# Kernel tuning notes

Hardware: AMD Instinct MI355X
Metric: run time of the kernel (lower is better)

Reference implementation:

```python
import jax, jax.numpy as jnp
import numpy as np

ROPE_BASE = 1000.0  # note: module uses base=1000, not the usual 10000


def _rope(x):
    # x: [B, L, H, d]; rotates the full head dim (x_pass is empty since d == hid_head)
    d = x.shape[-1]
    L = x.shape[1]
    theta = 1.0 / (ROPE_BASE ** (jnp.arange(0, d, 2, dtype=jnp.float32) / d))  # [d/2]
    idx = jnp.arange(L, dtype=jnp.float32)[:, None] * theta[None, :]            # [L, d/2]
    idx2 = jnp.concatenate([idx, idx], axis=-1)                                 # [L, d]
    cos = jnp.cos(idx2)[:, None, :]  # [L, 1, d] -> broadcasts over B, H
    sin = jnp.sin(idx2)[:, None, :]
    half = d // 2
    neg_half = jnp.concatenate([-x[..., half:], x[..., :half]], axis=-1)
    return x * cos + neg_half * sin


def setup_inputs() -> dict:
    key = jax.random.key(0)
    ks = jax.random.split(key, 8)
    B, Lq, Lc, F = 4, 1024, 2047, 2048
    s = 0.02
    return {
        "kv": jax.random.normal(ks[0], (B, 1, F), jnp.float32),
        "q": jax.random.normal(ks[1], (B, Lq, F), jnp.float32),
        "kv_cache": jax.random.normal(ks[2], (B, Lc, F, 2), jnp.float32),
        "Wq": jax.random.normal(ks[3], (F, F), jnp.float32) * s,
        "Wk": jax.random.normal(ks[4], (F, F), jnp.float32) * s,
        "Wv": jax.random.normal(ks[5], (F, F), jnp.float32) * s,
        "Wo": jax.random.normal(ks[6], (F, F), jnp.float32) * s,
        "mask": jnp.ones((B, 1, Lq, Lc + 1), jnp.int32),
        "num_heads": 16,
    }


def reference(kv, q, kv_cache, Wq, Wk, Wv, Wo, mask, num_heads):
    B = q.shape[0]
    F = Wq.shape[1]
    hd = F // num_heads

    query = q @ Wq                          # [B, Lq, F]
    key_new = kv[:, -1, :] @ Wk             # [B, F] (only last kv token is projected)
    val_new = kv[:, -1, :] @ Wv             # [B, F]

    key = jnp.concatenate([kv_cache[..., 0], key_new[:, None, :]], axis=1)    # [B, Lk, F]
    value = jnp.concatenate([kv_cache[..., 1], val_new[:, None, :]], axis=1)  # [B, Lk, F]
    kv_cache_out = jnp.stack([key, value], axis=-1)                            # [B, Lk, F, 2]

    query = query.reshape(B, -1, num_heads, hd)   # [B, Lq, H, d]
    key = key.reshape(B, -1, num_heads, hd)       # [B, Lk, H, d]
    value = value.reshape(B, -1, num_heads, hd)   # [B, Lk, H, d]

    query = _rope(query)
    key = _rope(key)

    aw = jnp.einsum('bqhd,bkhd->bhqk', query, key) / jnp.sqrt(jnp.float32(hd))
    aw = jnp.where(mask > 0, aw, -jnp.inf)  # mask [B,1,Lq,Lk] broadcasts over heads
    aw = jax.nn.softmax(aw, axis=-1)

    out = jnp.einsum('bhqk,bkhd->bqhd', aw, value).reshape(B, -1, F)
    logits = out @ Wo
    return logits, kv_cache_out
```

## Files before the change

### kernel.cpp

```cpp
#include <hip/hip_runtime.h>

#define B_  4
#define LQ  1024
#define LC  2047
#define LK  2048
#define F_  2048
#define H_  16
#define DH  128
#define NT  (LK / 64)

typedef __attribute__((ext_vector_type(4))) float f32x4;
typedef __attribute__((ext_vector_type(8))) __bf16 bf16x8;
typedef __attribute__((ext_vector_type(8))) unsigned short u16x8;

#define GLD16(gp, lp)                                                          \
  __builtin_amdgcn_global_load_lds(                                            \
      (const __attribute__((address_space(1))) void*)(gp),                     \
      (__attribute__((address_space(3))) void*)(lp), 16, 0, 0)

__device__ __forceinline__ unsigned short f2bf(float f) {
  unsigned u = __float_as_uint(f);
  u += 0x7FFFu + ((u >> 16) & 1u);
  return (unsigned short)(u >> 16);
}
__device__ __forceinline__ float bf2f(unsigned short u) {
  return __uint_as_float((unsigned)u << 16);
}
__device__ __forceinline__ unsigned pack_bf2(float a, float b) {
  return (__float_as_uint(b) & 0xffff0000u) | (__float_as_uint(a) >> 16);
}

__global__ void k_tables(float* __restrict__ cost, float* __restrict__ sint) {
  int idx = blockIdx.x * 256 + threadIdx.x;
  int pos = idx >> 6, j = idx & 63;
  float theta = powf(1000.0f, -(float)j / 64.0f);
  float a = (float)pos * theta;
  cost[idx] = cosf(a);
  sint[idx] = sinf(a);
}

__global__ void k_gemv_part(const float* __restrict__ kv, const float* __restrict__ Wk,
                            const float* __restrict__ Wv, float* __restrict__ part) {
  __shared__ float kvs[4][256];
  int tid = threadIdx.x, z = blockIdx.z;
#pragma unroll
  for (int b = 0; b < 4; ++b) kvs[b][tid] = kv[b * F_ + z * 256 + tid];
  __syncthreads();
  const float* W = blockIdx.y ? Wv : Wk;
  int col = blockIdx.x * 256 + tid;
  float a0 = 0.f, a1 = 0.f, a2 = 0.f, a3 = 0.f;
  for (int k = 0; k < 256; ++k) {
    float w = W[(size_t)(z * 256 + k) * F_ + col];
    a0 = fmaf(kvs[0][k], w, a0);
    a1 = fmaf(kvs[1][k], w, a1);
    a2 = fmaf(kvs[2][k], w, a2);
    a3 = fmaf(kvs[3][k], w, a3);
  }
  float* o = part + (size_t)(blockIdx.y * 8 + z) * 8192;
  o[col] = a0; o[2048 + col] = a1; o[4096 + col] = a2; o[6144 + col] = a3;
}

__global__ void k_prep_kv(const float* __restrict__ cache, const float* __restrict__ gpart,
                          const float* __restrict__ cost, const float* __restrict__ sint,
                          float* __restrict__ cache_out,
                          unsigned short* __restrict__ Kr, unsigned short* __restrict__ Vb) {
  int t = blockIdx.x * 256 + threadIdx.x;
  int j = t & 63, h = (t >> 6) & 15, pos = (t >> 10) & 2047, b = t >> 21;
  int f = h * DH + j;
  float k1, v1, k2, v2;
  if (pos < LC) {
    const float* p = cache + ((size_t)(b * LC + pos) * F_ + f) * 2;
    float2 x = *(const float2*)p;
    float2 y = *(const float2*)(p + 128);
    k1 = x.x; v1 = x.y; k2 = y.x; v2 = y.y;
  } else {
    float s0 = 0.f, s1 = 0.f, s2 = 0.f, s3 = 0.f;
#pragma unroll
    for (int z = 0; z < 8; ++z) {
      const float* gk = gpart + (size_t)z * 8192 + b * 2048;
      const float* gv = gpart + (size_t)(8 + z) * 8192 + b * 2048;
      s0 += gk[f]; s1 += gk[f + 64];
      s2 += gv[f]; s3 += gv[f + 64];
    }
    k1 = s0; k2 = s1; v1 = s2; v2 = s3;
  }
  float* o = cache_out + ((size_t)(b * LK + pos) * F_ + f) * 2;
  *(float2*)o = make_float2(k1, v1);
  *(float2*)(o + 128) = make_float2(k2, v2);
  float c = cost[pos * 64 + j], s = sint[pos * 64 + j];
  size_t kb = ((size_t)(b * H_ + h) * LK + pos) * DH + j;
  Kr[kb]      = f2bf(k1 * c - k2 * s);
  Kr[kb + 64] = f2bf(k2 * c + k1 * s);
  Vb[kb]      = f2bf(v1);
  Vb[kb + 64] = f2bf(v2);
}

__global__ void k_transpose_w(const float* __restrict__ Wq, const float* __restrict__ Wo,
                              unsigned short* __restrict__ WqT, unsigned short* __restrict__ WoT,
                              const float* __restrict__ qf, unsigned short* __restrict__ qb) {
  __shared__ float tile[32][33];
  int z = blockIdx.z;
  if (z >= 2) {
    int t = ((z - 2) * 4096 + blockIdx.y * 64 + blockIdx.x) * 256 + threadIdx.x;
    float4 v = ((const float4*)qf)[t];
    ushort4 o;
    o.x = f2bf(v.x); o.y = f2bf(v.y); o.z = f2bf(v.z); o.w = f2bf(v.w);
    ((ushort4*)qb)[t] = o;
    return;
  }
  const float* W = z ? Wo : Wq;
  unsigned short* Wt = z ? WoT : WqT;
  int n0 = blockIdx.x * 32, k0 = blockIdx.y * 32;
  int tx = threadIdx.x & 31, ty = threadIdx.x >> 5;
#pragma unroll
  for (int p = 0; p < 4; ++p)
    tile[ty + p * 8][tx] = W[(size_t)(k0 + ty + p * 8) * F_ + n0 + tx];
  __syncthreads();
#pragma unroll
  for (int p = 0; p < 4; ++p)
    Wt[(size_t)(n0 + ty + p * 8) * F_ + k0 + tx] = f2bf(tile[tx][ty + p * 8]);
}

template <int MODE>
__launch_bounds__(512)
__global__ void k_gemm(const unsigned short* __restrict__ A, const unsigned short* __restrict__ Bt,
                       void* __restrict__ Cv, const float* __restrict__ cost,
                       const float* __restrict__ sint, int M, int N, int K) {
  __shared__ __align__(16) unsigned short SM[49152];
  int tid = threadIdx.x, wid = tid >> 6, l = tid & 63;
  int wm = wid >> 1, wn = wid & 1;
  int lr = l & 15, lg = l >> 4;
  int m0 = blockIdx.y * 256, n0 = blockIdx.x * 128;

  int agoff[4], aloff[4], bgoff[2], bloff[2];
#pragma unroll
  for (int p = 0; p < 4; ++p) {
    int g = (p >> 1) * 1024 + (p & 1) * 512 + tid;
    int row = g >> 3, c = g & 7;
    agoff[p] = row * K + (c ^ (row & 7)) * 8;
    aloff[p] = g * 8;
  }
#pragma unroll
  for (int p = 0; p < 2; ++p) {
    int g = p * 512 + tid;
    int row = g >> 3, c = g & 7;
    bgoff[p] = row * K + (c ^ (row & 7)) * 8;
    bloff[p] = g * 8;
  }
  const unsigned short* Ag = A + (size_t)m0 * K;
  const unsigned short* Bg = Bt + (size_t)n0 * K;

  int fsw = (lr & 7);
  f32x4 acc[4][4];
#pragma unroll
  for (int i = 0; i < 4; ++i)
#pragma unroll
    for (int j = 0; j < 4; ++j) acc[i][j] = (f32x4){0.f, 0.f, 0.f, 0.f};

  int nk = K >> 6;
#pragma unroll
  for (int p = 0; p < 4; ++p) GLD16(Ag + agoff[p], SM + aloff[p]);
#pragma unroll
  for (int p = 0; p < 2; ++p) GLD16(Bg + bgoff[p], SM + 32768 + bloff[p]);

  for (int kt = 0; kt < nk; ++kt) {
    int cur = kt & 1;
    unsigned short* Ac = SM + cur * 16384;
    unsigned short* Bc = SM + 32768 + cur * 8192;
    unsigned short* An = SM + (cur ^ 1) * 16384;
    unsigned short* Bn = SM + 32768 + (cur ^ 1) * 8192;
    int knext = ((kt + 1 < nk) ? (kt + 1) : 0) << 6;

    __builtin_amdgcn_s_barrier();
    __builtin_amdgcn_sched_barrier(0);
    GLD16(Ag + knext + agoff[0], An + aloff[0]);
    GLD16(Ag + knext + agoff[1], An + aloff[1]);
    asm volatile("s_waitcnt vmcnt(2)" ::: "memory");
    __builtin_amdgcn_sched_barrier(0);
    __builtin_amdgcn_s_barrier();
    __builtin_amdgcn_sched_barrier(0);

    bf16x8 af[2][4], bf0[2];
#pragma unroll
    for (int kw = 0; kw < 2; ++kw)
#pragma unroll
      for (int mi = 0; mi < 4; ++mi)
        af[kw][mi] = *(const bf16x8*)&Ac[(wm * 64 + mi * 16 + lr) * 64 + (((kw * 4 + lg) ^ fsw) << 3)];
#pragma unroll
    for (int kw = 0; kw < 2; ++kw)
      bf0[kw] = *(const bf16x8*)&Bc[(wn * 64 + lr) * 64 + (((kw * 4 + lg) ^ fsw) << 3)];
    GLD16(Ag + knext + agoff[2], An + aloff[2]);
    GLD16(Ag + knext + agoff[3], An + aloff[3]);
    asm volatile("s_waitcnt lgkmcnt(0)" ::: "memory");
    __builtin_amdgcn_sched_barrier(0);
    __builtin_amdgcn_s_setprio(1);
#pragma unroll
    for (int kw = 0; kw < 2; ++kw)
#pragma unroll
      for (int mi = 0; mi < 4; ++mi)
        acc[mi][0] = __builtin_amdgcn_mfma_f32_16x16x32_bf16(af[kw][mi], bf0[kw], acc[mi][0], 0, 0, 0);
    __builtin_amdgcn_s_setprio(0);
    __builtin_amdgcn_s_barrier();

#pragma unroll
    for (int kw = 0; kw < 2; ++kw)
      bf0[kw] = *(const bf16x8*)&Bc[(wn * 64 + 16 + lr) * 64 + (((kw * 4 + lg) ^ fsw) << 3)];
    GLD16(Bg + knext + bgoff[0], Bn + bloff[0]);
    GLD16(Bg + knext + bgoff[1], Bn + bloff[1]);
    asm volatile("s_waitcnt lgkmcnt(0)" ::: "memory");
    __builtin_amdgcn_sched_barrier(0);
    __builtin_amdgcn_s_setprio(1);
#pragma unroll
    for (int kw = 0; kw < 2; ++kw)
#pragma unroll
      for (int mi = 0; mi < 4; ++mi)
        acc[mi][1] = __builtin_amdgcn_mfma_f32_16x16x32_bf16(af[kw][mi], bf0[kw], acc[mi][1], 0, 0, 0);
    __builtin_amdgcn_s_setprio(0);
    __builtin_amdgcn_s_barrier();

#pragma unroll
    for (int kw = 0; kw < 2; ++kw)
      bf0[kw] = *(const bf16x8*)&Bc[(wn * 64 + 32 + lr) * 64 + (((kw * 4 + lg) ^ fsw) << 3)];
    asm volatile("s_waitcnt lgkmcnt(0)" ::: "memory");
    __builtin_amdgcn_sched_barrier(0);
    __builtin_amdgcn_s_setprio(1);
#pragma unroll
    for (int kw = 0; kw < 2; ++kw)
#pragma unroll
      for (int mi = 0; mi < 4; ++mi)
        acc[mi][2] = __builtin_amdgcn_mfma_f32_16x16x32_bf16(af[kw][mi], bf0[kw], acc[mi][2], 0, 0, 0);
    __builtin_amdgcn_s_setprio(0);
    __builtin_amdgcn_s_barrier();

#pragma unroll
    for (int kw = 0; kw < 2; ++kw)
      bf0[kw] = *(const bf16x8*)&Bc[(wn * 64 + 48 + lr) * 64 + (((kw * 4 + lg) ^ fsw) << 3)];
    asm volatile("s_waitcnt lgkmcnt(0)" ::: "memory");
    __builtin_amdgcn_sched_barrier(0);
    __builtin_amdgcn_s_setprio(1);
#pragma unroll
    for (int kw = 0; kw < 2; ++kw)
#pragma unroll
      for (int mi = 0; mi < 4; ++mi)
        acc[mi][3] = __builtin_amdgcn_mfma_f32_16x16x32_bf16(af[kw][mi], bf0[kw], acc[mi][3], 0, 0, 0);
    __builtin_amdgcn_s_setprio(0);
  }
  asm volatile("s_waitcnt vmcnt(0)" ::: "memory");
  __syncthreads();

  if (MODE == 0) {
#pragma unroll
    for (int mi = 0; mi < 4; ++mi)
#pragma unroll
      for (int ni = 0; ni < 4; ++ni) {
        int row = m0 + wm * 64 + mi * 16 + lg * 4;
        int col = n0 + wn * 64 + ni * 16 + lr;
#pragma unroll
        for (int r = 0; r < 4; ++r)
          ((float*)Cv)[(size_t)(row + r) * N + col] = acc[mi][ni][r];
      }
  } else {
    unsigned short* X = SM;
#pragma unroll
    for (int mi = 0; mi < 4; ++mi)
#pragma unroll
      for (int ni = 0; ni < 4; ++ni) {
        int lrow = wm * 64 + mi * 16 + lg * 4;
        int col = wn * 64 + ni * 16 + lr;
#pragma unroll
        for (int r = 0; r < 4; ++r)
          X[(lrow + r) * 130 + col] = f2bf(acc[mi][ni][r]);
      }
    __syncthreads();
    int h = blockIdx.x;
    const float scale = 0.12751743343788055f;
    unsigned short* Q = (unsigned short*)Cv;
#pragma unroll
    for (int mi = 0; mi < 4; ++mi) {
      int lrow0 = wm * 64 + mi * 16 + lg * 4;
#pragma unroll
      for (int r = 0; r < 4; ++r) {
        int lrow = lrow0 + r;
        int grow = m0 + lrow;
        int qi = grow & 1023, b = grow >> 10;
        size_t obase = ((size_t)(b * H_ + h) * LQ + qi) * DH;
#pragma unroll
        for (int ni = 0; ni < 4; ++ni) {
          int col = wn * 64 + ni * 16 + lr;
          int jj = col & 63;
          float c = cost[qi * 64 + jj], s = sint[qi * 64 + jj];
          float a = acc[mi][ni][r];
          float a2 = bf2f(X[lrow * 130 + (col ^ 64)]);
          float o = (col < 64) ? (a * c - a2 * s) : (a * c + a2 * s);
          Q[obase + col] = f2bf(o * scale);
        }
      }
    }
  }
}

__launch_bounds__(256, 2)
__global__ void k_attn(const unsigned short* __restrict__ Qr, const unsigned short* __restrict__ Kr,
                       const unsigned short* __restrict__ Vb, unsigned short* __restrict__ Oo) {
  __shared__ __align__(16) unsigned short KsB[2][64 * 128];
  __shared__ __align__(16) unsigned short Vt[128][72];
  __shared__ __align__(16) unsigned short Pb[4][32][72];
  int tid = threadIdx.x, wid = tid >> 6, l = tid & 63;
  int lr = l & 15, lg = l >> 4;
  int bh = blockIdx.x, q0 = blockIdx.y * 128 + wid * 32;
  const unsigned short* Qb = Qr + ((size_t)bh * LQ + q0) * DH;
  const unsigned short* Kb = Kr + (size_t)bh * LK * DH;
  const unsigned short* Vp = Vb + (size_t)bh * LK * DH;

  bf16x8 qf[2][4];
#pragma unroll
  for (int s = 0; s < 2; ++s)
#pragma unroll
    for (int c = 0; c < 4; ++c)
      qf[s][c] = *(const bf16x8*)(Qb + (size_t)(s * 16 + lr) * DH + c * 32 + lg * 8);

  u16x8 one_u;
#pragma unroll
  for (int e = 0; e < 8; ++e) one_u[e] = 0x3F80;
  bf16x8 vone = *(const bf16x8*)&one_u;

  int gkoff[4], lkoff[4];
#pragma unroll
  for (int p = 0; p < 4; ++p) {
    int g = tid + p * 256, row = g >> 4, cc = g & 15;
    gkoff[p] = row * DH + (cc ^ (row & 15)) * 8;
    lkoff[p] = g * 8;
  }

  f32x4 oacc[2][8];
#pragma unroll
  for (int s = 0; s < 2; ++s)
#pragma unroll
    for (int i = 0; i < 8; ++i) oacc[s][i] = (f32x4){0.f, 0.f, 0.f, 0.f};
  f32x4 lacc[2] = {(f32x4){0.f, 0.f, 0.f, 0.f}, (f32x4){0.f, 0.f, 0.f, 0.f}};
  float mrun[2][4] = {{-1e30f, -1e30f, -1e30f, -1e30f}, {-1e30f, -1e30f, -1e30f, -1e30f}};

  int kp = tid >> 4, cg = tid & 15;

#pragma unroll
  for (int p = 0; p < 4; ++p) GLD16(Kb + gkoff[p], &KsB[0][lkoff[p]]);
  const unsigned short* vs0 = Vp + (size_t)kp * DH + cg * 8;
  u16x8 v00 = *(const u16x8*)(vs0);
  u16x8 v01 = *(const u16x8*)(vs0 + 16 * DH);
  u16x8 v10 = *(const u16x8*)(vs0 + 32 * DH);
  u16x8 v11 = *(const u16x8*)(vs0 + 48 * DH);

  for (int kt = 0; kt < NT; ++kt) {
    int cur = kt & 1;
    asm volatile("s_waitcnt vmcnt(0)" ::: "memory");
    __builtin_amdgcn_sched_barrier(0);
    __builtin_amdgcn_s_barrier();
    __builtin_amdgcn_sched_barrier(0);

#pragma unroll
    for (int pp = 0; pp < 2; ++pp) {
      int j = kp + pp * 16;
      int kks = j ^ ((cg & 7) << 2);
      u16x8 a = pp ? v10 : v00, b2 = pp ? v11 : v01;
#pragma unroll
      for (int e = 0; e < 8; ++e) {
        unsigned pack = (unsigned)a[e] | ((unsigned)b2[e] << 16);
        *(unsigned*)&Vt[cg * 8 + e][kks * 2] = pack;
      }
    }
    {
      const unsigned short* Kn = Kb + (size_t)((kt + 1 < NT) ? (kt + 1) * 64 * DH : 0);
#pragma unroll
      for (int p = 0; p < 4; ++p) GLD16(Kn + gkoff[p], &KsB[cur ^ 1][lkoff[p]]);
    }
    {
      int tn = (kt + 1 < NT) ? kt + 1 : kt;
      const unsigned short* vn = Vp + (size_t)(tn * 64 + kp) * DH + cg * 8;
      v00 = *(const u16x8*)(vn);
      v01 = *(const u16x8*)(vn + 16 * DH);
      v10 = *(const u16x8*)(vn + 32 * DH);
      v11 = *(const u16x8*)(vn + 48 * DH);
    }
    asm volatile("s_waitcnt lgkmcnt(0)" ::: "memory");
    __builtin_amdgcn_sched_barrier(0);
    __builtin_amdgcn_s_barrier();
    __builtin_amdgcn_sched_barrier(0);

    const unsigned short* Kcur = KsB[cur];
    f32x4 sf[2][4];
    __builtin_amdgcn_s_setprio(1);
#pragma unroll
    for (int ct = 0; ct < 4; ++ct) {
      f32x4 s0 = (f32x4){0.f, 0.f, 0.f, 0.f};
      f32x4 s1 = (f32x4){0.f, 0.f, 0.f, 0.f};
#pragma unroll
      for (int ck = 0; ck < 4; ++ck) {
        bf16x8 kf = *(const bf16x8*)&Kcur[(ct * 16 + lr) * 128 + (((ck * 4 + lg) ^ lr) << 3)];
        s0 = __builtin_amdgcn_mfma_f32_16x16x32_bf16(qf[0][ck], kf, s0, 0, 0, 0);
        s1 = __builtin_amdgcn_mfma_f32_16x16x32_bf16(qf[1][ck], kf, s1, 0, 0, 0);
      }
      sf[0][ct] = s0; sf[1][ct] = s1;
    }
    __builtin_amdgcn_s_setprio(0);

    float pmax[2][4];
    bool allok = true;
#pragma unroll
    for (int s = 0; s < 2; ++s)
#pragma unroll
      for (int r = 0; r < 4; ++r) {
        pmax[s][r] = fmaxf(fmaxf(sf[s][0][r], sf[s][1][r]), fmaxf(sf[s][2][r], sf[s][3][r]));
        allok = allok && (pmax[s][r] - mrun[s][r] <= 8.0f);
      }
    if (!__all(allok)) {
#pragma unroll
      for (int s = 0; s < 2; ++s)
#pragma unroll
        for (int r = 0; r < 4; ++r) {
          float m = pmax[s][r];
#pragma unroll
          for (int off = 1; off < 16; off <<= 1) m = fmaxf(m, __shfl_xor(m, off));
          float mnew = fmaxf(mrun[s][r], m);
          float scl = exp2f(mrun[s][r] - mnew);
          lacc[s][r] *= scl;
#pragma unroll
          for (int dt = 0; dt < 8; ++dt) oacc[s][dt][r] *= scl;
          mrun[s][r] = mnew;
        }
    }
#pragma unroll
    for (int s = 0; s < 2; ++s)
#pragma unroll
      for (int r = 0; r < 4; ++r) {
        float p0 = exp2f(sf[s][0][r] - mrun[s][r]);
        float p1 = exp2f(sf[s][1][r] - mrun[s][r]);
        float p2 = exp2f(sf[s][2][r] - mrun[s][r]);
        float p3 = exp2f(sf[s][3][r] - mrun[s][r]);
        unsigned* row = (unsigned*)&Pb[wid][s * 16 + lg * 4 + r][0];
        row[lr]      = pack_bf2(p0, p1);
        row[16 + lr] = pack_bf2(p2, p3);
      }

    bf16x8 pf00 = *(const bf16x8*)&Pb[wid][lr][lg * 8];
    bf16x8 pf01 = *(const bf16x8*)&Pb[wid][lr][32 + lg * 8];
    bf16x8 pf10 = *(const bf16x8*)&Pb[wid][16 + lr][lg * 8];
    bf16x8 pf11 = *(const bf16x8*)&Pb[wid][16 + lr][32 + lg * 8];
    __builtin_amdgcn_s_setprio(1);
    lacc[0] = __builtin_amdgcn_mfma_f32_16x16x32_bf16(pf00, vone, lacc[0], 0, 0, 0);
    lacc[0] = __builtin_amdgcn_mfma_f32_16x16x32_bf16(pf01, vone, lacc[0], 0, 0, 0);
    lacc[1] = __builtin_amdgcn_mfma_f32_16x16x32_bf16(pf10, vone, lacc[1], 0, 0, 0);
    lacc[1] = __builtin_amdgcn_mfma_f32_16x16x32_bf16(pf11, vone, lacc[1], 0, 0, 0);
#pragma unroll
    for (int dt = 0; dt < 8; ++dt) {
      int d = dt * 16 + lr;
      int x = (d >> 3) & 7;
      bf16x8 v0 = *(const bf16x8*)&Vt[d][(lg ^ x) << 3];
      bf16x8 v1 = *(const bf16x8*)&Vt[d][((4 + lg) ^ x) << 3];
      oacc[0][dt] = __builtin_amdgcn_mfma_f32_16x16x32_bf16(pf00, v0, oacc[0][dt], 0, 0, 0);
      oacc[0][dt] = __builtin_amdgcn_mfma_f32_16x16x32_bf16(pf01, v1, oacc[0][dt], 0, 0, 0);
      oacc[1][dt] = __builtin_amdgcn_mfma_f32_16x16x32_bf16(pf10, v0, oacc[1][dt], 0, 0, 0);
      oacc[1][dt] = __builtin_amdgcn_mfma_f32_16x16x32_bf16(pf11, v1, oacc[1][dt], 0, 0, 0);
    }
    __builtin_amdgcn_s_setprio(0);
  }

  int b = bh >> 4, h = bh & 15;
#pragma unroll
  for (int s = 0; s < 2; ++s)
#pragma unroll
    for (int r = 0; r < 4; ++r) {
      float inv = 1.0f / lacc[s][r];
      int qrow = q0 + s * 16 + lg * 4 + r;
      size_t base = ((size_t)(b * LQ + qrow)) * F_ + h * DH;
#pragma unroll
      for (int dt = 0; dt < 8; ++dt)
        Oo[base + dt * 16 + lr] = f2bf(oacc[s][dt][r] * inv);
    }
}

extern "C" void kernel_launch(void* const* d_in, const int* in_sizes, int n_in,
                              void* d_out, int out_size, void* d_ws, size_t ws_size,
                              hipStream_t stream) {
  const float* kv    = (const float*)d_in[0];
  const float* q     = (const float*)d_in[1];
  const float* cache = (const float*)d_in[2];
  const float* Wq    = (const float*)d_in[3];
  const float* Wk    = (const float*)d_in[4];
  const float* Wv    = (const float*)d_in[5];
  const float* Wo    = (const float*)d_in[6];

  float* logits    = (float*)d_out;
  float* cache_out = logits + (size_t)B_ * LQ * F_;

  char* ws = (char*)d_ws;
  float* cost          = (float*)(ws);
  float* sint          = (float*)(ws + 524288);
  float* gpart         = (float*)(ws + 1114112);
  unsigned short* WqT  = (unsigned short*)(ws + 1638400);
  unsigned short* WoT  = (unsigned short*)(ws + 10027008);
  unsigned short* qbf  = (unsigned short*)(ws + 18415616);
  unsigned short* Qro  = (unsigned short*)(ws + 35192832);
  unsigned short* Kro  = (unsigned short*)(ws + 51970048);
  unsigned short* Vbf  = (unsigned short*)(ws + 85524480);
  unsigned short* attno = (unsigned short*)(ws + 127467520);

  k_tables<<<dim3(512), dim3(256), 0, stream>>>(cost, sint);
  k_gemv_part<<<dim3(8, 2, 8), dim3(256), 0, stream>>>(kv, Wk, Wv, gpart);
  k_prep_kv<<<dim3(32768), dim3(256), 0, stream>>>(cache, gpart, cost, sint,
                                                   cache_out, Kro, Vbf);
  k_transpose_w<<<dim3(64, 64, 4), dim3(256), 0, stream>>>(Wq, Wo, WqT, WoT, q, qbf);
  k_gemm<2><<<dim3(16, 16), dim3(512), 0, stream>>>(qbf, WqT, Qro, cost, sint,
                                                    B_ * LQ, F_, F_);
  k_attn<<<dim3(64, 8), dim3(256), 0, stream>>>(Qro, Kro, Vbf, attno);
  k_gemm<0><<<dim3(16, 16), dim3(512), 0, stream>>>(attno, WoT, logits, nullptr, nullptr,
                                                    B_ * LQ, F_, F_);
}
```

Baseline: 276.3 us.

## Single-buffer K tile in attention for higher occupancy; widen prep_kv per-thread work

The attention kernel drops the double-buffered K shared-memory tile in favour of a single buffer. The K load is now issued at the top of each iteration and waited on with a partial vmcnt, and launch bounds rise from 2 to 3 blocks per CU. The goal is more resident waves to hide latency, at the cost of losing the K prefetch overlap inside each block. Separately, k_prep_kv now handles two adjacent features per thread with float4 loads and stores and packed bf16 writes, halving the grid to cut instruction and memory-transaction overhead.

```diff
diff --git a/kernel.cpp b/kernel.cpp
--- a/kernel.cpp
+++ b/kernel.cpp
@@ -28,6 +28,9 @@
 }
 __device__ __forceinline__ unsigned pack_bf2(float a, float b) {
   return (__float_as_uint(b) & 0xffff0000u) | (__float_as_uint(a) >> 16);
+}
+__device__ __forceinline__ unsigned pack_bf2_rne(float a, float b) {
+  return (unsigned)f2bf(a) | ((unsigned)f2bf(b) << 16);
 }
 
 __global__ void k_tables(float* __restrict__ cost, float* __restrict__ sint) {
@@ -65,34 +68,38 @@
                           float* __restrict__ cache_out,
                           unsigned short* __restrict__ Kr, unsigned short* __restrict__ Vb) {
   int t = blockIdx.x * 256 + threadIdx.x;
-  int j = t & 63, h = (t >> 6) & 15, pos = (t >> 10) & 2047, b = t >> 21;
-  int f = h * DH + j;
-  float k1, v1, k2, v2;
+  int j2 = t & 31, h = (t >> 5) & 15, pos = (t >> 9) & 2047, b = t >> 20;
+  int f = h * DH + j2 * 2;
+  float4 x, y;
   if (pos < LC) {
     const float* p = cache + ((size_t)(b * LC + pos) * F_ + f) * 2;
-    float2 x = *(const float2*)p;
-    float2 y = *(const float2*)(p + 128);
-    k1 = x.x; v1 = x.y; k2 = y.x; v2 = y.y;
+    x = *(const float4*)p;
+    y = *(const float4*)(p + 128);
   } else {
-    float s0 = 0.f, s1 = 0.f, s2 = 0.f, s3 = 0.f;
+    float k0 = 0, v0 = 0, k1 = 0, v1 = 0, k2 = 0, v2 = 0, k3 = 0, v3 = 0;
 #pragma unroll
     for (int z = 0; z < 8; ++z) {
       const float* gk = gpart + (size_t)z * 8192 + b * 2048;
       const float* gv = gpart + (size_t)(8 + z) * 8192 + b * 2048;
-      s0 += gk[f]; s1 += gk[f + 64];
-      s2 += gv[f]; s3 += gv[f + 64];
-    }
-    k1 = s0; k2 = s1; v1 = s2; v2 = s3;
+      k0 += gk[f];      k1 += gk[f + 1];
+      k2 += gk[f + 64]; k3 += gk[f + 65];
+      v0 += gv[f];      v1 += gv[f + 1];
+      v2 += gv[f + 64]; v3 += gv[f + 65];
+    }
+    x = make_float4(k0, v0, k1, v1);
+    y = make_float4(k2, v2, k3, v3);
   }
   float* o = cache_out + ((size_t)(b * LK + pos) * F_ + f) * 2;
-  *(float2*)o = make_float2(k1, v1);
-  *(float2*)(o + 128) = make_float2(k2, v2);
-  float c = cost[pos * 64 + j], s = sint[pos * 64 + j];
+  *(float4*)o = x;
+  *(float4*)(o + 128) = y;
+  int j = j2 * 2;
+  float c0 = cost[pos * 64 + j],     s0 = sint[pos * 64 + j];
+  float c1 = cost[pos * 64 + j + 1], s1 = sint[pos * 64 + j + 1];
   size_t kb = ((size_t)(b * H_ + h) * LK + pos) * DH + j;
-  Kr[kb]      = f2bf(k1 * c - k2 * s);
-  Kr[kb + 64] = f2bf(k2 * c + k1 * s);
-  Vb[kb]      = f2bf(v1);
-  Vb[kb + 64] = f2bf(v2);
+  *(unsigned*)&Kr[kb]      = pack_bf2_rne(x.x * c0 - y.x * s0, x.z * c1 - y.z * s1);
+  *(unsigned*)&Kr[kb + 64] = pack_bf2_rne(y.x * c0 + x.x * s0, y.z * c1 + x.z * s1);
+  *(unsigned*)&Vb[kb]      = pack_bf2_rne(x.y, x.w);
+  *(unsigned*)&Vb[kb + 64] = pack_bf2_rne(y.y, y.w);
 }
 
 __global__ void k_transpose_w(const float* __restrict__ Wq, const float* __restrict__ Wo,
@@ -299,10 +306,10 @@
   }
 }
 
-__launch_bounds__(256, 2)
+__launch_bounds__(256, 3)
 __global__ void k_attn(const unsigned short* __restrict__ Qr, const unsigned short* __restrict__ Kr,
                        const unsigned short* __restrict__ Vb, unsigned short* __restrict__ Oo) {
-  __shared__ __align__(16) unsigned short KsB[2][64 * 128];
+  __shared__ __align__(16) unsigned short Ks[64 * 128];
   __shared__ __align__(16) unsigned short Vt[128][72];
   __shared__ __align__(16) unsigned short Pb[4][32][72];
   int tid = threadIdx.x, wid = tid >> 6, l = tid & 63;
@@ -342,8 +349,6 @@
 
   int kp = tid >> 4, cg = tid & 15;
 
-#pragma unroll
-  for (int p = 0; p < 4; ++p) GLD16(Kb + gkoff[p], &KsB[0][lkoff[p]]);
   const unsigned short* vs0 = Vp + (size_t)kp * DH + cg * 8;
   u16x8 v00 = *(const u16x8*)(vs0);
   u16x8 v01 = *(const u16x8*)(vs0 + 16 * DH);
@@ -351,12 +356,13 @@
   u16x8 v11 = *(const u16x8*)(vs0 + 48 * DH);
 
   for (int kt = 0; kt < NT; ++kt) {
-    int cur = kt & 1;
-    asm volatile("s_waitcnt vmcnt(0)" ::: "memory");
-    __builtin_amdgcn_sched_barrier(0);
-    __builtin_amdgcn_s_barrier();
-    __builtin_amdgcn_sched_barrier(0);
-
+    __builtin_amdgcn_s_barrier();
+    __builtin_amdgcn_sched_barrier(0);
+    {
+      const unsigned short* Kt = Kb + (size_t)kt * 64 * DH;
+#pragma unroll
+      for (int p = 0; p < 4; ++p) GLD16(Kt + gkoff[p], Ks + lkoff[p]);
+    }
 #pragma unroll
     for (int pp = 0; pp < 2; ++pp) {
       int j = kp + pp * 16;
@@ -367,11 +373,6 @@
         unsigned pack = (unsigned)a[e] | ((unsigned)b2[e] << 16);
         *(unsigned*)&Vt[cg * 8 + e][kks * 2] = pack;
       }
-    }
-    {
-      const unsigned short* Kn = Kb + (size_t)((kt + 1 < NT) ? (kt + 1) * 64 * DH : 0);
-#pragma unroll
-      for (int p = 0; p < 4; ++p) GLD16(Kn + gkoff[p], &KsB[cur ^ 1][lkoff[p]]);
     }
     {
       int tn = (kt + 1 < NT) ? kt + 1 : kt;
@@ -381,12 +382,11 @@
       v10 = *(const u16x8*)(vn + 32 * DH);
       v11 = *(const u16x8*)(vn + 48 * DH);
     }
-    asm volatile("s_waitcnt lgkmcnt(0)" ::: "memory");
-    __builtin_amdgcn_sched_barrier(0);
-    __builtin_amdgcn_s_barrier();
-    __builtin_amdgcn_sched_barrier(0);
-
-    const unsigned short* Kcur = KsB[cur];
+    asm volatile("s_waitcnt vmcnt(4) lgkmcnt(0)" ::: "memory");
+    __builtin_amdgcn_sched_barrier(0);
+    __builtin_amdgcn_s_barrier();
+    __builtin_amdgcn_sched_barrier(0);
+
     f32x4 sf[2][4];
     __builtin_amdgcn_s_setprio(1);
 #pragma unroll
@@ -395,7 +395,7 @@
       f32x4 s1 = (f32x4){0.f, 0.f, 0.f, 0.f};
 #pragma unroll
       for (int ck = 0; ck < 4; ++ck) {
-        bf16x8 kf = *(const bf16x8*)&Kcur[(ct * 16 + lr) * 128 + (((ck * 4 + lg) ^ lr) << 3)];
+        bf16x8 kf = *(const bf16x8*)&Ks[(ct * 16 + lr) * 128 + (((ck * 4 + lg) ^ lr) << 3)];
         s0 = __builtin_amdgcn_mfma_f32_16x16x32_bf16(qf[0][ck], kf, s0, 0, 0, 0);
         s1 = __builtin_amdgcn_mfma_f32_16x16x32_bf16(qf[1][ck], kf, s1, 0, 0, 0);
       }
@@ -506,7 +506,7 @@
 
   k_tables<<<dim3(512), dim3(256), 0, stream>>>(cost, sint);
   k_gemv_part<<<dim3(8, 2, 8), dim3(256), 0, stream>>>(kv, Wk, Wv, gpart);
-  k_prep_kv<<<dim3(32768), dim3(256), 0, stream>>>(cache, gpart, cost, sint,
+  k_prep_kv<<<dim3(16384), dim3(256), 0, stream>>>(cache, gpart, cost, sint,
                                                    cache_out, Kro, Vbf);
   k_transpose_w<<<dim3(64, 64, 4), dim3(256), 0, stream>>>(Wq, Wo, WqT, WoT, q, qbf);
   k_gemm<2><<<dim3(16, 16), dim3(512), 0, stream>>>(qbf, WqT, Qro, cost, sint,
```

Result: slower. 484.3 us (+75.3%).
